# Kernel tuning notes

Measured on AMD Instinct MI355X. Metric: run time of the kernel, lower is better.

Reference implementation:

```python
import jax, jax.numpy as jnp
import numpy as np

IMAGE_SIZE = 128
FACES_PER_PIXEL = 4
BLUR_RADIUS = 0.01
EPS = 1e-8


def setup_inputs() -> dict:
    key = jax.random.key(0)
    k1, k2, k3 = jax.random.split(key, 3)
    B, V, F = 2, 2000, 800
    # verts are already projected to screen/NDC space: x,y in [-1,1], z > 0 (depth)
    xy = jax.random.uniform(k1, (B, V, 2), minval=-1.0, maxval=1.0)
    z = jax.random.uniform(k2, (B, V, 1), minval=0.5, maxval=2.5)
    verts = jnp.concatenate([xy, z], axis=-1).astype(jnp.float32)
    faces = jax.random.randint(k3, (F, 3), 0, V)
    return {"verts": verts, "faces": faces}


def _edge(a, b, p):
    # signed parallelogram area of (a -> b -> p), using xy components only
    return (p[..., 0] - a[..., 0]) * (b[..., 1] - a[..., 1]) - (
        p[..., 1] - a[..., 1]) * (b[..., 0] - a[..., 0])


def _seg_dist2(p, a, b):
    # squared distance from point p to segment [a, b] in 2D
    ab = b - a
    pa = p - a
    t = jnp.clip(jnp.sum(pa * ab, -1) / (jnp.sum(ab * ab, -1) + EPS), 0.0, 1.0)
    d = pa - t[..., None] * ab
    return jnp.sum(d * d, -1)


def _rasterize(verts, faces):
    H = W = IMAGE_SIZE
    K = FACES_PER_PIXEL
    B = verts.shape[0]
    fv = verts[:, faces]                      # [B,F,3,3] gather face vertices
    v0, v1, v2 = fv[:, :, 0], fv[:, :, 1], fv[:, :, 2]
    a0 = v0[:, None, :, :2]                   # [B,1,F,2]
    a1 = v1[:, None, :, :2]
    a2 = v2[:, None, :, :2]
    z0 = v0[:, None, :, 2]                    # [B,1,F]
    z1 = v1[:, None, :, 2]
    z2 = v2[:, None, :, 2]
    # pixel centers in NDC, pytorch3d convention: index 0 -> +1, last -> -1
    xs = 1.0 - 2.0 * (jnp.arange(W, dtype=verts.dtype) + 0.5) / W
    ys = 1.0 - 2.0 * (jnp.arange(H, dtype=verts.dtype) + 0.5) / H
    yy, xx = jnp.meshgrid(ys, xs, indexing="ij")
    p = jnp.stack([xx, yy], -1).reshape(1, -1, 1, 2)   # [1,P,1,2], P=H*W

    area = _edge(a0, a1, a2)                  # [B,1,F] signed face area*2
    w0 = _edge(a1, a2, p)                     # [B,P,F]
    w1 = _edge(a2, a0, p)
    w2 = _edge(a0, a1, p)
    denom = jnp.where(jnp.abs(area) > EPS, area,
                      jnp.where(area >= 0, EPS, -EPS))
    b0, b1, b2 = w0 / denom, w1 / denom, w2 / denom
    zpix = b0 * z0 + b1 * z1 + b2 * z2        # [B,P,F] interpolated depth

    inside = (b0 >= 0) & (b1 >= 0) & (b2 >= 0)
    dmin = jnp.minimum(_seg_dist2(p, a0, a1),
                       jnp.minimum(_seg_dist2(p, a1, a2),
                                   _seg_dist2(p, a2, a0)))
    dsign = jnp.where(inside, -dmin, dmin)    # signed squared edge distance

    valid = (inside | (dmin < BLUR_RADIUS)) & (zpix > EPS) & (
        jnp.abs(area) > EPS)
    zcand = jnp.where(valid, zpix, jnp.inf)
    _, idx = jax.lax.top_k(-zcand, K)         # K nearest faces per pixel

    take = lambda x: jnp.take_along_axis(x, idx, axis=-1)
    sel_valid = take(valid)
    pix_to_face = jnp.where(sel_valid, idx, -1)
    zbuf = jnp.where(sel_valid, take(zpix), -1.0)
    bary = jnp.stack([b0, b1, b2], -1)        # [B,P,F,3]
    bsel = jnp.take_along_axis(bary, idx[..., None], axis=2)  # [B,P,K,3]
    bsel = jnp.where(sel_valid[..., None], bsel, -1.0)
    dsel = jnp.where(sel_valid, take(dsign), -1.0)

    return (pix_to_face.reshape(B, H, W, K),
            zbuf.reshape(B, H, W, K),
            bsel.reshape(B, H, W, K, 3),
            dsel.reshape(B, H, W, K))


def reference(verts, faces):
    # Fragments: (pix_to_face, zbuf, bary_coords, dists)
    return _rasterize(verts, faces)
```

## Files before the change

### kernel.cpp

```cpp
#include <hip/hip_runtime.h>

#define IMG   128
#define KF    4
#define NF    800
#define NV    2000
#define NB    2
#define EPSF  1e-8f
#define BLURF 0.01f
#define CULL_D2 0.0103f
#define HEXT    0.0547f
#define FARC    0.0102f

typedef unsigned long long u64;
#define INVK ((((u64)0x7f800000u) << 32) | 0xffffffffu)

#pragma clang fp contract(off)

__device__ __forceinline__ void ins4(u64& s0, u64& s1, u64& s2, u64& s3, u64 k) {
    bool c0 = k < s0, c1 = k < s1, c2 = k < s2, c3 = k < s3;
    s3 = c2 ? s2 : (c3 ? k : s3);
    s2 = c1 ? s1 : (c2 ? k : s2);
    s1 = c0 ? s0 : (c1 ? k : s1);
    s0 = c0 ? k  : s0;
}

__global__ __launch_bounds__(256) void raster_p0(
    const float* __restrict__ verts,
    const int*   __restrict__ faces,
    float4* __restrict__ cullr,
    float4* __restrict__ recr)
{
#pragma clang fp contract(off)
    int t = blockIdx.x * 256 + threadIdx.x;
    if (t >= NB * NF) return;
    int b = t / NF, f = t - b * NF;
    const float* vb = verts + b * NV * 3;
    int i0 = faces[3*f+0], i1 = faces[3*f+1], i2 = faces[3*f+2];
    float a0x = vb[3*i0], a0y = vb[3*i0+1], z0 = vb[3*i0+2];
    float a1x = vb[3*i1], a1y = vb[3*i1+1], z1 = vb[3*i1+2];
    float a2x = vb[3*i2], a2y = vb[3*i2+1], z2 = vb[3*i2+2];
    float area = (a2x - a0x) * (a1y - a0y) - (a2y - a0y) * (a1x - a0x);
    float aab  = fabsf(area);
    float denom = (aab > EPSF) ? area : (area >= 0.0f ? EPSF : -EPSF);
    float e0x = a2x - a1x, e0y = a2y - a1y;
    float e1x = a0x - a2x, e1y = a0y - a2y;
    float e2x = a1x - a0x, e2y = a1y - a0y;

    float4 bb;
    if (aab > EPSF) {
        bb.x = fminf(a0x, fminf(a1x, a2x)) - 0.101f;
        bb.y = fmaxf(a0x, fmaxf(a1x, a2x)) + 0.101f;
        bb.z = fminf(a0y, fminf(a1y, a2y)) - 0.101f;
        bb.w = fmaxf(a0y, fmaxf(a1y, a2y)) + 0.101f;
    } else {
        bb.x = 1e30f; bb.y = -1e30f; bb.z = 1e30f; bb.w = -1e30f;
    }
    float s = (area >= 0.0f) ? 1.0f : -1.0f;
    float4 E0, E1, E2;
    E0.x = s * e0y; E0.y = -s * e0x;
    E0.z = s * (a1y * e0x - a1x * e0y) + HEXT * (fabsf(e0x) + fabsf(e0y));
    E0.w = CULL_D2 * (e0x * e0x + e0y * e0y);
    E1.x = s * e1y; E1.y = -s * e1x;
    E1.z = s * (a2y * e1x - a2x * e1y) + HEXT * (fabsf(e1x) + fabsf(e1y));
    E1.w = CULL_D2 * (e1x * e1x + e1y * e1y);
    E2.x = s * e2y; E2.y = -s * e2x;
    E2.z = s * (a0y * e2x - a0x * e2y) + HEXT * (fabsf(e2x) + fabsf(e2y));
    E2.w = CULL_D2 * (e2x * e2x + e2y * e2y);
    float4* cq = &cullr[(size_t)t * 4];
    cq[0] = bb; cq[1] = E0; cq[2] = E1; cq[3] = E2;

    float4* r = &recr[(size_t)t * 5];
    r[0] = make_float4(a0x, a0y, a1x, a1y);
    r[1] = make_float4(a2x, a2y, e0x, e0y);
    r[2] = make_float4(e1x, e1y, e2x, e2y);
    r[3] = make_float4(z0, z1, z2, denom);
    r[4] = make_float4((e2x * e2x + e2y * e2y) + EPSF,
                       (e0x * e0x + e0y * e0y) + EPSF,
                       (e1x * e1x + e1y * e1y) + EPSF,
                       0.0f);
}

__global__ __launch_bounds__(256) void raster_p1(
    const float4* __restrict__ cullr,
    const float4* __restrict__ recr,
    u64*          __restrict__ part,
    int sh)
{
#pragma clang fp contract(off)
    __shared__ int sList[800];
    __shared__ u64 sK[2 * 4 * 64];
    __shared__ unsigned sWc[4];

    const int S     = 1 << sh;
    const int chunk = NF >> sh;
    const int tid   = threadIdx.x;
    const int wave  = tid >> 6;
    const int lane  = tid & 63;
    const int unit  = blockIdx.x;
    const int tile  = unit >> sh;
    const int slice = unit & (S - 1);
    const int b     = tile >> 8;
    const int trow  = (tile & 255) >> 4;
    const int tcol  = tile & 15;
    const int fbase = slice * chunk;

    const int pr = lane >> 3, pc = lane & 7;
    const int row = trow * 8 + pr, col = tcol * 8 + pc;
    const float px = 1.0f - (2.0f * ((float)col + 0.5f)) / 128.0f;
    const float py = 1.0f - (2.0f * ((float)row + 0.5f)) / 128.0f;
    const float txmax = 1.0f - (2.0f * ((float)(tcol * 8)     + 0.5f)) / 128.0f;
    const float txmin = 1.0f - (2.0f * ((float)(tcol * 8 + 7) + 0.5f)) / 128.0f;
    const float tymax = 1.0f - (2.0f * ((float)(trow * 8)     + 0.5f)) / 128.0f;
    const float tymin = 1.0f - (2.0f * ((float)(trow * 8 + 7) + 0.5f)) / 128.0f;
    const float cx = 0.5f * (txmin + txmax);
    const float cy = 0.5f * (tymin + tymax);

    int scnt = 0;
    for (int j0 = 0; j0 < chunk; j0 += 256) {
        const int jl = j0 + tid;
        bool surv = false;
        if (jl < chunk) {
            const int f = fbase + jl;
            const float4* cq = &cullr[(size_t)(b * NF + f) * 4];
            float4 bb = cq[0], E0 = cq[1], E1 = cq[2], E2 = cq[3];
            surv = !(bb.x > txmax || bb.y < txmin || bb.z > tymax || bb.w < tymin);
            float w0 = E0.x * cx + E0.y * cy + E0.z;
            float w1 = E1.x * cx + E1.y * cy + E1.z;
            float w2 = E2.x * cx + E2.y * cy + E2.z;
            surv &= !((w0 < 0.0f) & (w0 * w0 > E0.w));
            surv &= !((w1 < 0.0f) & (w1 * w1 > E1.w));
            surv &= !((w2 < 0.0f) & (w2 * w2 > E2.w));
        }
        u64 m = __ballot(surv);
        if (lane == 0) sWc[wave] = (unsigned)__popcll(m);
        __syncthreads();
        int off = scnt;
        for (int w = 0; w < 4; ++w) { if (w < wave) off += (int)sWc[w]; }
        int tot = (int)(sWc[0] + sWc[1] + sWc[2] + sWc[3]);
        if (surv) sList[off + __popcll(m & ((1ull << lane) - 1ull))] = fbase + jl;
        scnt += tot;
        __syncthreads();
    }

    u64 s0 = INVK, s1 = INVK, s2 = INVK, s3 = INVK;
    for (int j = wave; j < scnt; j += 4) {
        const int fg = sList[j];
        const float4* r = &recr[(size_t)(b * NF + fg) * 5];
        float4 q0 = r[0], q1 = r[1], q2 = r[2], q3 = r[3], q4 = r[4];
        float a0x=q0.x, a0y=q0.y, a1x=q0.z, a1y=q0.w, a2x=q1.x, a2y=q1.y;
        float e0x=q1.z, e0y=q1.w, e1x=q2.x, e1y=q2.y, e2x=q2.z, e2y=q2.w;
        float z0=q3.x, z1=q3.y, z2=q3.z, D=q3.w;
        float ddA=q4.x, ddB=q4.y, ddC=q4.z;
        float p0x = px - a0x, p0y = py - a0y;
        float p1x = px - a1x, p1y = py - a1y;
        float p2x = px - a2x, p2y = py - a2y;
        float w0 = p1x * e0y - p1y * e0x;
        float w1 = p2x * e1y - p2y * e1x;
        float w2 = p0x * e2y - p0y * e2x;
        float b0 = w0 / D, b1 = w1 / D, b2 = w2 / D;
        float zpix = (b0 * z0 + b1 * z1) + b2 * z2;
        bool inside = fminf(b0, fminf(b1, b2)) >= 0.0f;
        bool far = (w0 * w0 > FARC * ddB) & (w1 * w1 > FARC * ddC) & (w2 * w2 > FARC * ddA);
        bool valid;
        if (__all(inside | far)) {
            valid = inside & (zpix > EPSF);
        } else {
            float tA = (p0x * e2x + p0y * e2y) / ddA;
            tA = fminf(fmaxf(tA, 0.0f), 1.0f);
            float dxA = p0x - tA * e2x, dyA = p0y - tA * e2y;
            float dA = dxA * dxA + dyA * dyA;
            float tB = (p1x * e0x + p1y * e0y) / ddB;
            tB = fminf(fmaxf(tB, 0.0f), 1.0f);
            float dxB = p1x - tB * e0x, dyB = p1y - tB * e0y;
            float dB = dxB * dxB + dyB * dyB;
            float tC = (p2x * e1x + p2y * e1y) / ddC;
            tC = fminf(fmaxf(tC, 0.0f), 1.0f);
            float dxC = p2x - tC * e1x, dyC = p2y - tC * e1y;
            float dC = dxC * dxC + dyC * dyC;
            float dmin = fminf(dA, fminf(dB, dC));
            valid = (inside | (dmin < BLURF)) & (zpix > EPSF);
        }
        u64 key = valid ? ((((u64)__float_as_uint(zpix)) << 32) | (unsigned)fg) : INVK;
        if (__any(key < s3)) ins4(s0, s1, s2, s3, key);
    }

    if (wave >= 2) {
        int r = wave - 2;
        sK[(r * 4 + 0) * 64 + lane] = s0;
        sK[(r * 4 + 1) * 64 + lane] = s1;
        sK[(r * 4 + 2) * 64 + lane] = s2;
        sK[(r * 4 + 3) * 64 + lane] = s3;
    }
    __syncthreads();
    if (wave < 2) {
        ins4(s0, s1, s2, s3, sK[(wave * 4 + 0) * 64 + lane]);
        ins4(s0, s1, s2, s3, sK[(wave * 4 + 1) * 64 + lane]);
        ins4(s0, s1, s2, s3, sK[(wave * 4 + 2) * 64 + lane]);
        ins4(s0, s1, s2, s3, sK[(wave * 4 + 3) * 64 + lane]);
    }
    __syncthreads();
    if (wave == 1) {
        sK[0 * 64 + lane] = s0;
        sK[1 * 64 + lane] = s1;
        sK[2 * 64 + lane] = s2;
        sK[3 * 64 + lane] = s3;
    }
    __syncthreads();
    if (wave == 0) {
        ins4(s0, s1, s2, s3, sK[0 * 64 + lane]);
        ins4(s0, s1, s2, s3, sK[1 * 64 + lane]);
        ins4(s0, s1, s2, s3, sK[2 * 64 + lane]);
        ins4(s0, s1, s2, s3, sK[3 * 64 + lane]);
        u64* wrow = part + (size_t)unit * 256;
        wrow[0 * 64 + lane] = s0;
        wrow[1 * 64 + lane] = s1;
        wrow[2 * 64 + lane] = s2;
        wrow[3 * 64 + lane] = s3;
    }
}

__global__ __launch_bounds__(256) void raster_p2(
    const float* __restrict__ verts,
    const int*   __restrict__ faces,
    const u64* __restrict__ part,
    int sh,
    float* __restrict__ out0, float* __restrict__ out1,
    float* __restrict__ out2, float* __restrict__ out3)
{
#pragma clang fp contract(off)
    __shared__ u64 sK[4 * 64];
    const int S    = 1 << sh;
    const int tid  = threadIdx.x;
    const int tile = blockIdx.x;
    const int b    = tile >> 8;
    const int trow = (tile & 255) >> 4;
    const int tcol = tile & 15;
    const float* vb = verts + b * NV * 3;

    if (tid < 64) {
        u64 s0 = INVK, s1 = INVK, s2 = INVK, s3 = INVK;
        const u64* base = part + (size_t)tile * S * 256;
        for (int s = 0; s < S; ++s) {
            ins4(s0, s1, s2, s3, base[s * 256 + 0 * 64 + tid]);
            ins4(s0, s1, s2, s3, base[s * 256 + 1 * 64 + tid]);
            ins4(s0, s1, s2, s3, base[s * 256 + 2 * 64 + tid]);
            ins4(s0, s1, s2, s3, base[s * 256 + 3 * 64 + tid]);
        }
        sK[0 * 64 + tid] = s0;
        sK[1 * 64 + tid] = s1;
        sK[2 * 64 + tid] = s2;
        sK[3 * 64 + tid] = s3;
    }
    __syncthreads();

    int pix = tid >> 2, k = tid & 3;
    u64 key = sK[k * 64 + pix];
    int prow = pix >> 3, pcol = pix & 7;
    int grow = trow * 8 + prow, gcol = tcol * 8 + pcol;
    int p = (b * IMG + grow) * IMG + gcol;
    float qx = 1.0f - (2.0f * ((float)gcol + 0.5f)) / 128.0f;
    float qy = 1.0f - (2.0f * ((float)grow + 0.5f)) / 128.0f;
    float o0 = -1.0f, o1 = -1.0f, ob0 = -1.0f, ob1 = -1.0f, ob2 = -1.0f, o3 = -1.0f;
    if ((unsigned)(key >> 32) != 0x7f800000u) {
        int fi = (int)(unsigned)(key & 0xffffffffu);
        int i0 = faces[3 * fi + 0], i1 = faces[3 * fi + 1], i2 = faces[3 * fi + 2];
        float a0x = vb[3 * i0], a0y = vb[3 * i0 + 1], z0 = vb[3 * i0 + 2];
        float a1x = vb[3 * i1], a1y = vb[3 * i1 + 1], z1 = vb[3 * i1 + 2];
        float a2x = vb[3 * i2], a2y = vb[3 * i2 + 1], z2 = vb[3 * i2 + 2];
        float area = (a2x - a0x) * (a1y - a0y) - (a2y - a0y) * (a1x - a0x);
        float aab  = fabsf(area);
        float denom = (aab > EPSF) ? area : (area >= 0.0f ? EPSF : -EPSF);
        float e0x = a2x - a1x, e0y = a2y - a1y;
        float e1x = a0x - a2x, e1y = a0y - a2y;
        float e2x = a1x - a0x, e2y = a1y - a0y;
        float p0x = qx - a0x, p0y = qy - a0y;
        float p1x = qx - a1x, p1y = qy - a1y;
        float p2x = qx - a2x, p2y = qy - a2y;
        float w0 = p1x * e0y - p1y * e0x;
        float w1 = p2x * e1y - p2y * e1x;
        float w2 = p0x * e2y - p0y * e2x;
        float b0 = w0 / denom, b1 = w1 / denom, b2 = w2 / denom;
        float zpix = (b0 * z0 + b1 * z1) + b2 * z2;
        bool inside = (b0 >= 0.0f) & (b1 >= 0.0f) & (b2 >= 0.0f);
        float ddA = (e2x * e2x + e2y * e2y) + EPSF;
        float tA = (p0x * e2x + p0y * e2y) / ddA;
        tA = fminf(fmaxf(tA, 0.0f), 1.0f);
        float dxA = p0x - tA * e2x, dyA = p0y - tA * e2y;
        float dA = dxA * dxA + dyA * dyA;
        float ddB = (e0x * e0x + e0y * e0y) + EPSF;
        float tB = (p1x * e0x + p1y * e0y) / ddB;
        tB = fminf(fmaxf(tB, 0.0f), 1.0f);
        float dxB = p1x - tB * e0x, dyB = p1y - tB * e0y;
        float dB = dxB * dxB + dyB * dyB;
        float ddC = (e1x * e1x + e1y * e1y) + EPSF;
        float tC = (p2x * e1x + p2y * e1y) / ddC;
        tC = fminf(fmaxf(tC, 0.0f), 1.0f);
        float dxC = p2x - tC * e1x, dyC = p2y - tC * e1y;
        float dC = dxC * dxC + dyC * dyC;
        float dmin = fminf(dA, fminf(dB, dC));
        o0 = (float)fi;
        o1 = zpix;
        ob0 = b0; ob1 = b1; ob2 = b2;
        o3 = inside ? -dmin : dmin;
    }
    int o = p * KF + k;
    out0[o] = o0;
    out1[o] = o1;
    out2[o * 3 + 0] = ob0;
    out2[o * 3 + 1] = ob1;
    out2[o * 3 + 2] = ob2;
    out3[o] = o3;
}

extern "C" void kernel_launch(void* const* d_in, const int* in_sizes, int n_in,
                              void* d_out, int out_size, void* d_ws, size_t ws_size,
                              hipStream_t stream) {
    const float* verts = (const float*)d_in[0];
    const int*   faces = (const int*)d_in[1];
    float* out = (float*)d_out;
    const int n0 = NB * IMG * IMG * KF;

    float4* cullr = (float4*)d_ws;
    float4* recr  = (float4*)((char*)d_ws + 102400);
    u64*    part  = (u64*)((char*)d_ws + 262144);

    const size_t per_unit = 256 * sizeof(u64);
    int sh = (ws_size >= 262144 + (512ull << 2) * per_unit) ? 2 : 0;
    const int S = 1 << sh;

    raster_p0<<<dim3((NB * NF + 255) / 256), dim3(256), 0, stream>>>(verts, faces, cullr, recr);
    raster_p1<<<dim3(512 * S), dim3(256), 0, stream>>>(cullr, recr, part, sh);
    raster_p2<<<dim3(512), dim3(256), 0, stream>>>(verts, faces, part, sh,
        out,
        out + n0,
        out + 2 * n0,
        out + 5 * n0);
}
```

Baseline: 98.93 us.

## Stage surviving face records in shared memory and split faces across more slices

The cull pass now copies each surviving face's full 20-float record into dynamic shared memory, packing the face index into the spare slot. The per-pixel loop then reads records from LDS with one-iteration software prefetch instead of gathering them from global memory through an index list. The slice count rises from 4 to 8 (or 2 as fallback), so each block handles 100 faces in a single cull pass. This doubles the partial-result writes and the merge work in p2, and it assumes chunk ≤ 256, which breaks if sh falls back to 0.

```diff
diff --git a/kernel.cpp b/kernel.cpp
--- a/kernel.cpp
+++ b/kernel.cpp
@@ -10,6 +10,7 @@
 #define CULL_D2 0.0103f
 #define HEXT    0.0547f
 #define FARC    0.0102f
+#define REC     20
 
 typedef unsigned long long u64;
 #define INVK ((((u64)0x7f800000u) << 32) | 0xffffffffu)
@@ -87,7 +88,7 @@
     int sh)
 {
 #pragma clang fp contract(off)
-    __shared__ int sList[800];
+    extern __shared__ float sREC[];
     __shared__ u64 sK[2 * 4 * 64];
     __shared__ unsigned sWc[4];
 
@@ -115,42 +116,62 @@
     const float cx = 0.5f * (txmin + txmax);
     const float cy = 0.5f * (tymin + tymax);
 
-    int scnt = 0;
-    for (int j0 = 0; j0 < chunk; j0 += 256) {
-        const int jl = j0 + tid;
-        bool surv = false;
-        if (jl < chunk) {
-            const int f = fbase + jl;
-            const float4* cq = &cullr[(size_t)(b * NF + f) * 4];
-            float4 bb = cq[0], E0 = cq[1], E1 = cq[2], E2 = cq[3];
-            surv = !(bb.x > txmax || bb.y < txmin || bb.z > tymax || bb.w < tymin);
-            float w0 = E0.x * cx + E0.y * cy + E0.z;
-            float w1 = E1.x * cx + E1.y * cy + E1.z;
-            float w2 = E2.x * cx + E2.y * cy + E2.z;
-            surv &= !((w0 < 0.0f) & (w0 * w0 > E0.w));
-            surv &= !((w1 < 0.0f) & (w1 * w1 > E1.w));
-            surv &= !((w2 < 0.0f) & (w2 * w2 > E2.w));
+    bool surv = false;
+    if (tid < chunk) {
+        const int gf = b * NF + fbase + tid;
+        const float4* cq = &cullr[(size_t)gf * 4];
+        float4 bb = cq[0], E0 = cq[1], E1 = cq[2], E2 = cq[3];
+        surv = !(bb.x > txmax || bb.y < txmin || bb.z > tymax || bb.w < tymin);
+        float w0 = E0.x * cx + E0.y * cy + E0.z;
+        float w1 = E1.x * cx + E1.y * cy + E1.z;
+        float w2 = E2.x * cx + E2.y * cy + E2.z;
+        surv &= !((w0 < 0.0f) & (w0 * w0 > E0.w));
+        surv &= !((w1 < 0.0f) & (w1 * w1 > E1.w));
+        surv &= !((w2 < 0.0f) & (w2 * w2 > E2.w));
+    }
+    u64 m = __ballot(surv);
+    if (lane == 0) sWc[wave] = (unsigned)__popcll(m);
+    __syncthreads();
+    int off = 0;
+    for (int w = 0; w < 4; ++w) { if (w < wave) off += (int)sWc[w]; }
+    const int scnt = (int)(sWc[0] + sWc[1] + sWc[2] + sWc[3]);
+    if (surv) {
+        int pos = off + __popcll(m & ((1ull << lane) - 1ull));
+        const float4* r = &recr[(size_t)(b * NF + fbase + tid) * 5];
+        float4 q0 = r[0], q1 = r[1], q2 = r[2], q3 = r[3], q4 = r[4];
+        q4.w = __int_as_float(fbase + tid);
+        float* d = &sREC[pos * REC];
+        *(float4*)(d)      = q0;
+        *(float4*)(d + 4)  = q1;
+        *(float4*)(d + 8)  = q2;
+        *(float4*)(d + 12) = q3;
+        *(float4*)(d + 16) = q4;
+    }
+    __syncthreads();
+
+    u64 s0 = INVK, s1 = INVK, s2 = INVK, s3 = INVK;
+    int j = wave;
+    float4 c0, c1, c2, c3, c4;
+    if (j < scnt) {
+        const float* r = &sREC[j * REC];
+        c0 = *(const float4*)(r);      c1 = *(const float4*)(r + 4);
+        c2 = *(const float4*)(r + 8);  c3 = *(const float4*)(r + 12);
+        c4 = *(const float4*)(r + 16);
+    }
+    while (j < scnt) {
+        const int jn = j + 4;
+        float4 n0 = c0, n1 = c1, n2 = c2, n3 = c3, n4 = c4;
+        if (jn < scnt) {
+            const float* r = &sREC[jn * REC];
+            n0 = *(const float4*)(r);      n1 = *(const float4*)(r + 4);
+            n2 = *(const float4*)(r + 8);  n3 = *(const float4*)(r + 12);
+            n4 = *(const float4*)(r + 16);
         }
-        u64 m = __ballot(surv);
-        if (lane == 0) sWc[wave] = (unsigned)__popcll(m);
-        __syncthreads();
-        int off = scnt;
-        for (int w = 0; w < 4; ++w) { if (w < wave) off += (int)sWc[w]; }
-        int tot = (int)(sWc[0] + sWc[1] + sWc[2] + sWc[3]);
-        if (surv) sList[off + __popcll(m & ((1ull << lane) - 1ull))] = fbase + jl;
-        scnt += tot;
-        __syncthreads();
-    }
-
-    u64 s0 = INVK, s1 = INVK, s2 = INVK, s3 = INVK;
-    for (int j = wave; j < scnt; j += 4) {
-        const int fg = sList[j];
-        const float4* r = &recr[(size_t)(b * NF + fg) * 5];
-        float4 q0 = r[0], q1 = r[1], q2 = r[2], q3 = r[3], q4 = r[4];
-        float a0x=q0.x, a0y=q0.y, a1x=q0.z, a1y=q0.w, a2x=q1.x, a2y=q1.y;
-        float e0x=q1.z, e0y=q1.w, e1x=q2.x, e1y=q2.y, e2x=q2.z, e2y=q2.w;
-        float z0=q3.x, z1=q3.y, z2=q3.z, D=q3.w;
-        float ddA=q4.x, ddB=q4.y, ddC=q4.z;
+        float a0x=c0.x, a0y=c0.y, a1x=c0.z, a1y=c0.w, a2x=c1.x, a2y=c1.y;
+        float e0x=c1.z, e0y=c1.w, e1x=c2.x, e1y=c2.y, e2x=c2.z, e2y=c2.w;
+        float z0=c3.x, z1=c3.y, z2=c3.z, D=c3.w;
+        float ddA=c4.x, ddB=c4.y, ddC=c4.z;
+        int   fg = __float_as_int(c4.w);
         float p0x = px - a0x, p0y = py - a0y;
         float p1x = px - a1x, p1y = py - a1y;
         float p2x = px - a2x, p2y = py - a2y;
@@ -182,6 +203,8 @@
         }
         u64 key = valid ? ((((u64)__float_as_uint(zpix)) << 32) | (unsigned)fg) : INVK;
         if (__any(key < s3)) ins4(s0, s1, s2, s3, key);
+        j = jn;
+        c0 = n0; c1 = n1; c2 = n2; c3 = n3; c4 = n4;
     }
 
     if (wave >= 2) {
@@ -325,11 +348,13 @@
     u64*    part  = (u64*)((char*)d_ws + 262144);
 
     const size_t per_unit = 256 * sizeof(u64);
-    int sh = (ws_size >= 262144 + (512ull << 2) * per_unit) ? 2 : 0;
+    int sh = (ws_size >= 262144 + (512ull << 3) * per_unit) ? 3 : 2;
     const int S = 1 << sh;
+    const int chunk = NF >> sh;
+    const size_t dyn = (size_t)chunk * REC * sizeof(float);
 
     raster_p0<<<dim3((NB * NF + 255) / 256), dim3(256), 0, stream>>>(verts, faces, cullr, recr);
-    raster_p1<<<dim3(512 * S), dim3(256), 0, stream>>>(cullr, recr, part, sh);
+    raster_p1<<<dim3(512 * S), dim3(256), dyn, stream>>>(cullr, recr, part, sh);
     raster_p2<<<dim3(512), dim3(256), 0, stream>>>(verts, faces, part, sh,
         out,
         out + n0,
```

Result: no change. 100.4 us (+1.4%).
